# Kernel optimization log

Hardware: AMD Instinct MI355X
Metric: run time of the kernel (lower is better)

## Reference

```python
import jax, jax.numpy as jnp
import numpy as np

H, W = 256, 256
N = 1024
EPS2D = 1e-4  # regularizer added to 2D covariances before inversion


def setup_inputs() -> dict:
    key = jax.random.key(0)
    ks = jax.random.split(key, 6)
    xy = jax.random.normal(ks[0], (N, 2), dtype=jnp.float32) * 3.0
    z = jax.random.uniform(ks[1], (N, 1), minval=2.0, maxval=30.0, dtype=jnp.float32)
    means3D = jnp.concatenate([xy, z], axis=-1)                      # [N,3], depths in (1,50)
    A = 0.1 * jax.random.normal(ks[2], (N, 3, 3), dtype=jnp.float32)
    covs3d = A @ jnp.swapaxes(A, -1, -2) + 0.01 * jnp.eye(3, dtype=jnp.float32)  # SPD [N,3,3]
    colors = jax.random.uniform(ks[3], (N, 3), dtype=jnp.float32)
    opacities = jax.random.uniform(ks[4], (N,), dtype=jnp.float32)
    Kmat = jnp.array([[300.0, 0.0, W / 2.0], [0.0, 300.0, H / 2.0], [0.0, 0.0, 1.0]], dtype=jnp.float32)
    Rmat = jnp.eye(3, dtype=jnp.float32)
    t = jnp.zeros((3,), dtype=jnp.float32)
    return {"means3D": means3D, "covs3d": covs3d, "colors": colors,
            "opacities": opacities, "K": Kmat, "R": Rmat, "t": t}


def reference(means3D, covs3d, colors, opacities, K, R, t):
    n = means3D.shape[0]
    # ---- projection ----
    cam = means3D @ R.T + t[None, :]                      # [N,3]
    depths = jnp.maximum(cam[:, 2], 1.0)
    screen = cam @ K.T
    means2D = screen[:, :2] / screen[:, 2:3]              # [N,2]
    fx, fy = K[0, 0], K[1, 1]
    inv_z = 1.0 / cam[:, 2]
    z2 = cam[:, 2] ** 2
    zeros = jnp.zeros_like(inv_z)
    row0 = jnp.stack([inv_z * fx, zeros, -cam[:, 0] / z2 * fx], axis=-1)
    row1 = jnp.stack([zeros, inv_z * fy, -cam[:, 1] / z2 * fy], axis=-1)
    J = jnp.stack([row0, row1], axis=1)                   # [N,2,3]
    covs_cam = jnp.einsum('ij,njk,lk->nil', R, covs3d, R)  # [N,3,3]
    covs2D = jnp.einsum('nij,njk,nlk->nil', J, covs_cam, J)  # [N,2,2]

    # ---- depth sort ----
    order = jnp.argsort(depths)
    means2D = means2D[order]
    covs2D = covs2D[order]
    colors_s = colors[order]
    opac_s = opacities[order]
    depths_s = depths[order]
    valid = (depths_s > 1.0) & (depths_s < 50.0)

    # ---- per-pixel gaussian evaluation (closed-form 2x2 inverse == cholesky_inverse) ----
    covs2D = covs2D + EPS2D * jnp.eye(2, dtype=covs2D.dtype)
    a = covs2D[:, 0, 0]; b = covs2D[:, 0, 1]; c = covs2D[:, 1, 1]
    det = a * c - b * b                                   # [N]
    ia = c / det; ib = -b / det; ic = a / det

    yy, xx = jnp.meshgrid(jnp.arange(H, dtype=jnp.float32),
                          jnp.arange(W, dtype=jnp.float32), indexing='ij')
    dx0 = xx[None] - means2D[:, 0, None, None]            # [N,H,W]
    dx1 = yy[None] - means2D[:, 1, None, None]            # [N,H,W]
    q = (ia[:, None, None] * dx0 * dx0
         + 2.0 * ib[:, None, None] * dx0 * dx1
         + ic[:, None, None] * dx1 * dx1)
    gauss = jnp.exp(-0.5 * q) / (2.0 * jnp.pi * jnp.sqrt(det))[:, None, None]
    gauss = gauss * valid[:, None, None].astype(gauss.dtype)

    # ---- alpha compositing (front-to-back) ----
    alphas = opac_s[:, None, None] * gauss                # [N,H,W]
    T = jnp.cumprod(1.0 - alphas, axis=0)
    T = jnp.concatenate([jnp.ones_like(alphas[:1]), T[:-1]], axis=0)
    weights = T * alphas                                  # [N,H,W]
    rendered = jnp.einsum('nhw,nc->hwc', weights, colors_s)  # [H,W,3]
    return rendered
```

## Files before the change

### kernel.cpp

```cpp
#include <hip/hip_runtime.h>
#include <math.h>

#define HH 256
#define WW 256
#define EPS2D 1e-4f
#define MAXN 1024
#define CULL_THR 23.0f
#define NL_HALF_LOG2E -0.72134752044448170368f


__global__ __launch_bounds__(256) void prep_kernel(
    const float* __restrict__ means3D, const float* __restrict__ covs3d,
    const float* __restrict__ colors,  const float* __restrict__ opac,
    const float* __restrict__ Km,      const float* __restrict__ Rm,
    const float* __restrict__ tv,
    float4* __restrict__ A, float4* __restrict__ B, float* __restrict__ C,
    int n)
{
    __shared__ float s_mean[MAXN*3];
    __shared__ float s_depth[MAXN];
    __shared__ float s_cov[64*9];
    __shared__ float s_col[64*3];
    __shared__ float s_op[64];
    __shared__ int   s_pr[4][64];

    int t = threadIdx.x, lane = t & 63, w = t >> 6;
    int g0b = blockIdx.x * 64;
    int nb = n - g0b; if (nb > 64) nb = 64; if (nb < 0) nb = 0;

    {
        int nm4 = (3*n) >> 2;
        const float4* m4 = (const float4*)means3D;
        for (int i = t; i < nm4; i += 256) ((float4*)s_mean)[i] = m4[i];
        for (int i = (nm4<<2) + t; i < 3*n; i += 256) s_mean[i] = means3D[i];

        const float* cbase = covs3d + (size_t)g0b * 9;
        int ncf = nb * 9, nc4 = ncf >> 2;
        for (int i = t; i < nc4; i += 256) ((float4*)s_cov)[i] = ((const float4*)cbase)[i];
        for (int i = (nc4<<2) + t; i < ncf; i += 256) s_cov[i] = cbase[i];

        const float* lbase = colors + (size_t)g0b * 3;
        int nlf = nb * 3, nl4 = nlf >> 2;
        for (int i = t; i < nl4; i += 256) ((float4*)s_col)[i] = ((const float4*)lbase)[i];
        for (int i = (nl4<<2) + t; i < nlf; i += 256) s_col[i] = lbase[i];

        const float* obase = opac + g0b;
        int no4 = nb >> 2;
        for (int i = t; i < no4; i += 256) ((float4*)s_op)[i] = ((const float4*)obase)[i];
        for (int i = (no4<<2) + t; i < nb; i += 256) s_op[i] = obase[i];
    }
    __syncthreads();

    float R00=Rm[0],R01=Rm[1],R02=Rm[2];
    float R10=Rm[3],R11=Rm[4],R12=Rm[5];
    float R20=Rm[6],R21=Rm[7],R22=Rm[8];
    float t0=tv[0], t1=tv[1], t2=tv[2];

    for (int g = t; g < MAXN; g += 256) {
        float d = 1e30f;
        if (g < n) {
            float X=s_mean[3*g+0], Y=s_mean[3*g+1], Z=s_mean[3*g+2];
            float cz = R20*X + R21*Y + R22*Z + t2;
            d = fmaxf(cz, 1.0f);
        }
        s_depth[g] = d;
    }
    __syncthreads();

    float mx=0.f,my=0.f,qa=0.f,qb=0.f,qc=0.f,lk=0.f,cr=0.f,cg=0.f,cbv=0.f;
    if (w == 0 && lane < nb) {
        int i = g0b + lane;
        float X = s_mean[3*i+0], Y = s_mean[3*i+1], Z = s_mean[3*i+2];
        float cx = R00*X + R01*Y + R02*Z + t0;
        float cy = R10*X + R11*Y + R12*Z + t1;
        float cz = R20*X + R21*Y + R22*Z + t2;
        float depth = s_depth[i];

        float K00=Km[0],K01=Km[1],K02=Km[2];
        float K10=Km[3],K11=Km[4],K12=Km[5];
        float K20=Km[6],K21=Km[7],K22=Km[8];
        float sx = K00*cx + K01*cy + K02*cz;
        float sy = K10*cx + K11*cy + K12*cz;
        float sz = K20*cx + K21*cy + K22*cz;
        mx = sx / sz;
        my = sy / sz;

        float fx = K00, fy = K11;
        float invz  = 1.0f / cz;
        float invz2 = invz * invz;
        float j00 =  fx * invz;
        float j02 = -fx * cx * invz2;
        float j11 =  fy * invz;
        float j12 = -fy * cy * invz2;

        const float* S = s_cov + 9*lane;
        float S00=S[0],S01=S[1],S02=S[2];
        float S10=S[3],S11=S[4],S12=S[5];
        float S20=S[6],S21=S[7],S22=S[8];

        float M00 = R00*S00 + R01*S10 + R02*S20;
        float M01 = R00*S01 + R01*S11 + R02*S21;
        float M02 = R00*S02 + R01*S12 + R02*S22;
        float M10 = R10*S00 + R11*S10 + R12*S20;
        float M11 = R10*S01 + R11*S11 + R12*S21;
        float M12 = R10*S02 + R11*S12 + R12*S22;
        float M20 = R20*S00 + R21*S10 + R22*S20;
        float M21 = R20*S01 + R21*S11 + R22*S21;
        float M22 = R20*S02 + R21*S12 + R22*S22;
        float C00 = M00*R00 + M01*R01 + M02*R02;
        float C01 = M00*R10 + M01*R11 + M02*R12;
        float C02 = M00*R20 + M01*R21 + M02*R22;
        float C11 = M10*R10 + M11*R11 + M12*R12;
        float C12 = M10*R20 + M11*R21 + M12*R22;
        float C22 = M20*R20 + M21*R21 + M22*R22;

        float a_ = j00*j00*C00 + 2.0f*j00*j02*C02 + j02*j02*C22 + EPS2D;
        float b_ = j00*j11*C01 + j00*j12*C02 + j02*j11*C12 + j02*j12*C22;
        float c_ = j11*j11*C11 + 2.0f*j11*j12*C12 + j12*j12*C22 + EPS2D;

        float det = a_ * c_ - b_ * b_;
        float ia =  c_ / det;
        float ib = -b_ / det;
        float ic =  a_ / det;
        float norm = 1.0f / (6.283185307179586f * sqrtf(det));

        bool valid = (depth > 1.0f) && (depth < 50.0f);
        float k = s_op[lane] * norm * (valid ? 1.0f : 0.0f);

        qa = NL_HALF_LOG2E * ia;
        qb = 2.0f * NL_HALF_LOG2E * ib;
        qc = NL_HALF_LOG2E * ic;
        lk = log2f(k);
        cr = s_col[3*lane+0];
        cg = s_col[3*lane+1];
        cbv = s_col[3*lane+2];
    }

    {
        int cnt = 0;
        if (lane < nb) {
            int i = g0b + lane;
            float d = s_depth[i];
            const float4* d4 = (const float4*)s_depth;
            int jb = w * 64;
            #pragma unroll 4
            for (int jj = 0; jj < 64; ++jj) {
                float4 v = d4[jb + jj];
                int j = (jb + jj) << 2;
                cnt += (v.x < d || (v.x == d && j+0 < i)) ? 1 : 0;
                cnt += (v.y < d || (v.y == d && j+1 < i)) ? 1 : 0;
                cnt += (v.z < d || (v.z == d && j+2 < i)) ? 1 : 0;
                cnt += (v.w < d || (v.w == d && j+3 < i)) ? 1 : 0;
            }
        }
        s_pr[w][lane] = cnt;
    }
    __syncthreads();

    if (w == 0 && lane < nb) {
        int rank = s_pr[0][lane] + s_pr[1][lane] + s_pr[2][lane] + s_pr[3][lane];
        A[rank] = make_float4(mx, my, qa, qb);
        B[rank] = make_float4(qc, lk, cr, cg);
        C[rank] = cbv;
    }
}

__global__ __launch_bounds__(256) void render_kernel(
    const float4* __restrict__ A, const float4* __restrict__ B,
    const float* __restrict__ C, float* __restrict__ out, int n)
{
    __shared__ int    s_idx[4][256];
    __shared__ float4 s_p0[4][64];
    __shared__ float4 s_p1[4][64];
    __shared__ float4 s_part[3][256];

    int t = threadIdx.x, lane = t & 63, w = t >> 6;
    int row = blockIdx.x;
    int q0 = (n *  w     ) >> 2;
    int q1 = (n * (w + 1)) >> 2;
    float pyf = (float)row;

    int cnt = 0;
    if (q1 > q0) {
        int jc = min(q0 + lane, q1 - 1);
        float4 a = A[jc];
        float4 b = B[jc];
        for (int c = q0; c < q1; c += 64) {
            float4 a_n, b_n;
            int cn = c + 64;
            if (cn < q1) {
                int jc2 = min(cn + lane, q1 - 1);
                a_n = A[jc2];
                b_n = B[jc2];
            }
            int jj = c + lane;
            bool keep = false;
            if (jj < q1) {
                float cc = b.y + CULL_THR;
                if (cc > 0.0f) {
                    float dpp = fmaf(4.0f*a.z, b.x, -a.w*a.w);
                    float inv = cc / dpp;
                    float dxe = sqrtf(fmaxf(-4.0f*b.x*inv, 0.0f));
                    float dye = sqrtf(fmaxf(-4.0f*a.z*inv, 0.0f));
                    keep = (a.x + dxe >= 0.0f) && (a.x - dxe <= 255.0f) &&
                           (a.y + dye >= pyf)  && (a.y - dye <= pyf);
                }
            }
            unsigned long long mk = __ballot(keep);
            int pre = __popcll(mk & ((1ull << lane) - 1ull));
            if (keep) s_idx[w][cnt + pre] = jj;
            cnt += __popcll(mk);
            a = a_n; b = b_n;
        }
    }

    float lanef = (float)lane;
    float T0=1.f,T1=1.f,T2=1.f,T3=1.f;
    float r0=0.f,g0=0.f,b0=0.f, r1=0.f,g1=0.f,b1=0.f;
    float r2=0.f,g2=0.f,b2=0.f, r3=0.f,g3=0.f,b3=0.f;

    for (int k0 = 0; k0 < cnt; k0 += 64) {
        int m = cnt - k0; if (m > 64) m = 64;
        if (lane < m) {
            int jj = s_idx[w][k0 + lane];
            float4 a  = A[jj];
            float4 bb = B[jj];
            float  cc = C[jj];
            float dy = pyf - a.y;
            s_p0[w][lane] = make_float4(a.x, a.z, a.w * dy,
                                        fmaf(bb.x * dy, dy, bb.y));
            s_p1[w][lane] = make_float4(bb.z, bb.w, cc, 0.f);
        }
        for (int k = 0; k < m; ++k) {
            float4 p0 = s_p0[w][k];
            float4 p1 = s_p1[w][k];
            float dx = lanef - p0.x;
            {
                float q = fmaf(fmaf(p0.y, dx, p0.z), dx, p0.w);
                float wg = T0 * __builtin_amdgcn_exp2f(q);
                r0 = fmaf(wg, p1.x, r0); g0 = fmaf(wg, p1.y, g0);
                b0 = fmaf(wg, p1.z, b0); T0 -= wg;
            }
            dx += 64.0f;
            {
                float q = fmaf(fmaf(p0.y, dx, p0.z), dx, p0.w);
                float wg = T1 * __builtin_amdgcn_exp2f(q);
                r1 = fmaf(wg, p1.x, r1); g1 = fmaf(wg, p1.y, g1);
                b1 = fmaf(wg, p1.z, b1); T1 -= wg;
            }
            dx += 64.0f;
            {
                float q = fmaf(fmaf(p0.y, dx, p0.z), dx, p0.w);
                float wg = T2 * __builtin_amdgcn_exp2f(q);
                r2 = fmaf(wg, p1.x, r2); g2 = fmaf(wg, p1.y, g2);
                b2 = fmaf(wg, p1.z, b2); T2 -= wg;
            }
            dx += 64.0f;
            {
                float q = fmaf(fmaf(p0.y, dx, p0.z), dx, p0.w);
                float wg = T3 * __builtin_amdgcn_exp2f(q);
                r3 = fmaf(wg, p1.x, r3); g3 = fmaf(wg, p1.y, g3);
                b3 = fmaf(wg, p1.z, b3); T3 -= wg;
            }
        }
    }

    if (w != 0) {
        s_part[w-1][lane +   0] = make_float4(r0, g0, b0, T0);
        s_part[w-1][lane +  64] = make_float4(r1, g1, b1, T1);
        s_part[w-1][lane + 128] = make_float4(r2, g2, b2, T2);
        s_part[w-1][lane + 192] = make_float4(r3, g3, b3, T3);
    }
    __syncthreads();
    if (w == 0) {
        float rr[4] = {r0, r1, r2, r3};
        float gg[4] = {g0, g1, g2, g3};
        float bbv[4] = {b0, b1, b2, b3};
        float tt[4] = {T0, T1, T2, T3};
        #pragma unroll
        for (int i = 0; i < 4; ++i) {
            int px = lane + (i << 6);
            float4 m1 = s_part[0][px];
            float4 m2 = s_part[1][px];
            float4 m3 = s_part[2][px];
            float cr = m2.x + m2.w * m3.x;
            float cg = m2.y + m2.w * m3.y;
            float cb = m2.z + m2.w * m3.z;
            cr = m1.x + m1.w * cr;
            cg = m1.y + m1.w * cg;
            cb = m1.z + m1.w * cb;
            cr = rr[i] + tt[i] * cr;
            cg = gg[i] + tt[i] * cg;
            cb = bbv[i] + tt[i] * cb;
            int p = row * 256 + px;
            out[3*p+0] = cr;
            out[3*p+1] = cg;
            out[3*p+2] = cb;
        }
    }
}

extern "C" void kernel_launch(void* const* d_in, const int* in_sizes, int n_in,
                              void* d_out, int out_size, void* d_ws, size_t ws_size,
                              hipStream_t stream)
{
    const float* means3D = (const float*)d_in[0];
    const float* covs3d  = (const float*)d_in[1];
    const float* colors  = (const float*)d_in[2];
    const float* opac    = (const float*)d_in[3];
    const float* Km      = (const float*)d_in[4];
    const float* Rm      = (const float*)d_in[5];
    const float* tv      = (const float*)d_in[6];
    int n = in_sizes[3];
    if (n > MAXN) n = MAXN;

    float4* A = (float4*)d_ws;
    float4* B = (float4*)((char*)d_ws + 16384);
    float*  C = (float*)((char*)d_ws + 32768);

    int pblocks = (n + 63) / 64;
    hipLaunchKernelGGL(prep_kernel, dim3(pblocks), dim3(256), 0, stream,
                       means3D, covs3d, colors, opac, Km, Rm, tv, A, B, C, n);

    hipLaunchKernelGGL(render_kernel, dim3(HH), dim3(256), 0, stream,
                       A, B, C, (float*)d_out, n);
}
```

Measured before the change: 23.85 us.

## Write culled splat params directly to LDS and tighten per-row culling

The culling pass now computes the per-row quadratic coefficients during the scan and writes the full per-gaussian parameters straight into per-wave LDS buffers sized for the whole quarter. This removes the index list, the second gather from global memory and the chunked staging loop in compositing. The cull test changes from a bounding ellipse box to the exact x-interval of the ellipse on the current row, which should keep fewer gaussians. LDS use grows (two 4x256 float4 arrays), which may lower occupancy.

```diff
diff --git a/kernel.cpp b/kernel.cpp
--- a/kernel.cpp
+++ b/kernel.cpp
@@ -85,13 +85,12 @@
         mx = sx / sz;
         my = sy / sz;
 
-        float fx = K00, fy = K11;
         float invz  = 1.0f / cz;
         float invz2 = invz * invz;
-        float j00 =  fx * invz;
-        float j02 = -fx * cx * invz2;
-        float j11 =  fy * invz;
-        float j12 = -fy * cy * invz2;
+        float j00 =  K00 * invz;
+        float j02 = -K00 * cx * invz2;
+        float j11 =  K11 * invz;
+        float j12 = -K11 * cy * invz2;
 
         const float* S = s_cov + 9*lane;
         float S00=S[0],S01=S[1],S02=S[2];
@@ -169,9 +168,8 @@
     const float4* __restrict__ A, const float4* __restrict__ B,
     const float* __restrict__ C, float* __restrict__ out, int n)
 {
-    __shared__ int    s_idx[4][256];
-    __shared__ float4 s_p0[4][64];
-    __shared__ float4 s_p1[4][64];
+    __shared__ float4 s_p0[4][256];
+    __shared__ float4 s_p1[4][256];
     __shared__ float4 s_part[3][256];
 
     int t = threadIdx.x, lane = t & 63, w = t >> 6;
@@ -185,32 +183,42 @@
         int jc = min(q0 + lane, q1 - 1);
         float4 a = A[jc];
         float4 b = B[jc];
-        for (int c = q0; c < q1; c += 64) {
-            float4 a_n, b_n;
-            int cn = c + 64;
+        float  c = C[jc];
+        for (int ch = q0; ch < q1; ch += 64) {
+            float4 a_n, b_n; float c_n;
+            int cn = ch + 64;
             if (cn < q1) {
                 int jc2 = min(cn + lane, q1 - 1);
                 a_n = A[jc2];
                 b_n = B[jc2];
+                c_n = C[jc2];
             }
-            int jj = c + lane;
+            int jj = ch + lane;
             bool keep = false;
+            float qbdy = 0.f, u = 0.f;
             if (jj < q1) {
-                float cc = b.y + CULL_THR;
-                if (cc > 0.0f) {
-                    float dpp = fmaf(4.0f*a.z, b.x, -a.w*a.w);
-                    float inv = cc / dpp;
-                    float dxe = sqrtf(fmaxf(-4.0f*b.x*inv, 0.0f));
-                    float dye = sqrtf(fmaxf(-4.0f*a.z*inv, 0.0f));
-                    keep = (a.x + dxe >= 0.0f) && (a.x - dxe <= 255.0f) &&
-                           (a.y + dye >= pyf)  && (a.y - dye <= pyf);
+                float dy = pyf - a.y;
+                qbdy = a.w * dy;
+                u    = fmaf(b.x * dy, dy, b.y);
+                float disc = fmaf(qbdy, qbdy, -4.0f * a.z * (u + CULL_THR));
+                if (disc > 0.0f) {
+                    float inv2qa = 0.5f / a.z;
+                    float shw = sqrtf(disc) * inv2qa;
+                    float ctr = -qbdy * inv2qa;
+                    float xl = a.x + ctr + shw;
+                    float xr = a.x + ctr - shw;
+                    keep = (xr >= 0.0f) && (xl <= 255.0f);
                 }
             }
             unsigned long long mk = __ballot(keep);
             int pre = __popcll(mk & ((1ull << lane) - 1ull));
-            if (keep) s_idx[w][cnt + pre] = jj;
+            if (keep) {
+                int pos = cnt + pre;
+                s_p0[w][pos] = make_float4(a.x, a.z, qbdy, u);
+                s_p1[w][pos] = make_float4(b.z, b.w, c, 0.f);
+            }
             cnt += __popcll(mk);
-            a = a_n; b = b_n;
+            a = a_n; b = b_n; c = c_n;
         }
     }
 
@@ -219,49 +227,36 @@
     float r0=0.f,g0=0.f,b0=0.f, r1=0.f,g1=0.f,b1=0.f;
     float r2=0.f,g2=0.f,b2=0.f, r3=0.f,g3=0.f,b3=0.f;
 
-    for (int k0 = 0; k0 < cnt; k0 += 64) {
-        int m = cnt - k0; if (m > 64) m = 64;
-        if (lane < m) {
-            int jj = s_idx[w][k0 + lane];
-            float4 a  = A[jj];
-            float4 bb = B[jj];
-            float  cc = C[jj];
-            float dy = pyf - a.y;
-            s_p0[w][lane] = make_float4(a.x, a.z, a.w * dy,
-                                        fmaf(bb.x * dy, dy, bb.y));
-            s_p1[w][lane] = make_float4(bb.z, bb.w, cc, 0.f);
-        }
-        for (int k = 0; k < m; ++k) {
-            float4 p0 = s_p0[w][k];
-            float4 p1 = s_p1[w][k];
-            float dx = lanef - p0.x;
-            {
-                float q = fmaf(fmaf(p0.y, dx, p0.z), dx, p0.w);
-                float wg = T0 * __builtin_amdgcn_exp2f(q);
-                r0 = fmaf(wg, p1.x, r0); g0 = fmaf(wg, p1.y, g0);
-                b0 = fmaf(wg, p1.z, b0); T0 -= wg;
-            }
-            dx += 64.0f;
-            {
-                float q = fmaf(fmaf(p0.y, dx, p0.z), dx, p0.w);
-                float wg = T1 * __builtin_amdgcn_exp2f(q);
-                r1 = fmaf(wg, p1.x, r1); g1 = fmaf(wg, p1.y, g1);
-                b1 = fmaf(wg, p1.z, b1); T1 -= wg;
-            }
-            dx += 64.0f;
-            {
-                float q = fmaf(fmaf(p0.y, dx, p0.z), dx, p0.w);
-                float wg = T2 * __builtin_amdgcn_exp2f(q);
-                r2 = fmaf(wg, p1.x, r2); g2 = fmaf(wg, p1.y, g2);
-                b2 = fmaf(wg, p1.z, b2); T2 -= wg;
-            }
-            dx += 64.0f;
-            {
-                float q = fmaf(fmaf(p0.y, dx, p0.z), dx, p0.w);
-                float wg = T3 * __builtin_amdgcn_exp2f(q);
-                r3 = fmaf(wg, p1.x, r3); g3 = fmaf(wg, p1.y, g3);
-                b3 = fmaf(wg, p1.z, b3); T3 -= wg;
-            }
+    for (int k = 0; k < cnt; ++k) {
+        float4 p0 = s_p0[w][k];
+        float4 p1 = s_p1[w][k];
+        float dx = lanef - p0.x;
+        {
+            float q = fmaf(fmaf(p0.y, dx, p0.z), dx, p0.w);
+            float wg = T0 * __builtin_amdgcn_exp2f(q);
+            r0 = fmaf(wg, p1.x, r0); g0 = fmaf(wg, p1.y, g0);
+            b0 = fmaf(wg, p1.z, b0); T0 -= wg;
+        }
+        dx += 64.0f;
+        {
+            float q = fmaf(fmaf(p0.y, dx, p0.z), dx, p0.w);
+            float wg = T1 * __builtin_amdgcn_exp2f(q);
+            r1 = fmaf(wg, p1.x, r1); g1 = fmaf(wg, p1.y, g1);
+            b1 = fmaf(wg, p1.z, b1); T1 -= wg;
+        }
+        dx += 64.0f;
+        {
+            float q = fmaf(fmaf(p0.y, dx, p0.z), dx, p0.w);
+            float wg = T2 * __builtin_amdgcn_exp2f(q);
+            r2 = fmaf(wg, p1.x, r2); g2 = fmaf(wg, p1.y, g2);
+            b2 = fmaf(wg, p1.z, b2); T2 -= wg;
+        }
+        dx += 64.0f;
+        {
+            float q = fmaf(fmaf(p0.y, dx, p0.z), dx, p0.w);
+            float wg = T3 * __builtin_amdgcn_exp2f(q);
+            r3 = fmaf(wg, p1.x, r3); g3 = fmaf(wg, p1.y, g3);
+            b3 = fmaf(wg, p1.z, b3); T3 -= wg;
         }
     }
 
@@ -273,10 +268,10 @@
     }
     __syncthreads();
     if (w == 0) {
-        float rr[4] = {r0, r1, r2, r3};
-        float gg[4] = {g0, g1, g2, g3};
+        float rr[4]  = {r0, r1, r2, r3};
+        float gg[4]  = {g0, g1, g2, g3};
         float bbv[4] = {b0, b1, b2, b3};
-        float tt[4] = {T0, T1, T2, T3};
+        float tt[4]  = {T0, T1, T2, T3};
         #pragma unroll
         for (int i = 0; i < 4; ++i) {
             int px = lane + (i << 6);
```

New measurement: 23.48 us. Within noise of the previous version (-1.6%).
